# Performance work log

Measured on AMD Instinct MI355X. Metric: run time of the kernel, lower is better.

## Reference

```python
import jax, jax.numpy as jnp
import numpy as np

B, N, E, D = 4, 2048, 2048, 2048  # batch, seq, embedding_dim, out_dim


def setup_inputs() -> dict:
    key = jax.random.key(0)
    k1, k2, k3 = jax.random.split(key, 3)
    x = jax.random.normal(k1, (B, N, E), dtype=jnp.float32)
    # qkv_proj: Linear(E, 3*D). Store weight as [E, 3D] for x @ W.
    W = jax.random.normal(k2, (E, 3 * D), dtype=jnp.float32) * (1.0 / np.sqrt(E))
    b = jax.random.normal(k3, (3 * D,), dtype=jnp.float32) * 0.01
    return {"x": x, "W": W, "b": b}


def reference(x, W, b):
    d = W.shape[1] // 3
    n = x.shape[1]
    qkv = x @ W + b                                   # [B, N, 3D]
    q, k, v = jnp.split(qkv, 3, axis=-1)              # each [B, N, D]
    scale = 1.0 / np.sqrt(d).astype(np.float32)
    att = jnp.einsum('bqd,bkd->bqk', q, k) * scale    # [B, N, N]
    causal = jnp.tril(jnp.ones((n, n), dtype=bool))
    att = jnp.where(causal[None, :, :], att, -jnp.inf)
    # softmax_with_denom: stable softmax, also return the denominator
    m = jnp.max(att, axis=-1, keepdims=True)
    e = jnp.exp(att - m)
    denom = jnp.sum(e, axis=-1)                       # [B, N]
    p = e / denom[..., None]
    y = jnp.einsum('bqk,bkd->bqd', p, v)              # [B, N, D]
    return y, denom
```

## Files before the change

### kernel.cpp

```cpp
#include <hip/hip_runtime.h>

typedef unsigned short u16;
typedef unsigned int   u32;

#define SEQ 2048
#define EMB 2048
#define TD  6144

using bf16x8 = __attribute__((ext_vector_type(8))) __bf16;
using f32x4  = __attribute__((ext_vector_type(4))) float;
using u16x8v = __attribute__((ext_vector_type(8))) u16;

typedef __attribute__((address_space(1))) const void* gas_t;
typedef __attribute__((address_space(3))) void*       las_t;
#define GLOAD16(g, l) __builtin_amdgcn_global_load_lds((gas_t)(g), (las_t)(l), 16, 0, 0)

__device__ __forceinline__ u16 f2bf(float f) {
  u32 u = __float_as_uint(f);
  u += 0x7fffu + ((u >> 16) & 1u);
  return (u16)(u >> 16);
}
__device__ __forceinline__ float bf2f(u16 b) {
  u32 u = (u32)b << 16;
  return __uint_as_float(u);
}

__global__ __launch_bounds__(256) void prep_kern(const float* __restrict__ x,
                                                 u16* __restrict__ xb,
                                                 const float* __restrict__ W,
                                                 u16* __restrict__ Wt) {
  int bid = blockIdx.x;
  int tid = threadIdx.x;
  if (bid < 16384) {
    size_t i = ((size_t)bid * 256 + tid) * 4;
    float4 v = *(const float4*)(x + i);
    ushort4 u;
    u.x = f2bf(v.x); u.y = f2bf(v.y); u.z = f2bf(v.z); u.w = f2bf(v.w);
    *(ushort4*)(xb + i) = u;
  } else {
    __shared__ float t[64][65];
    int wb = bid - 16384;
    int c0 = (wb % 96) * 64, r0 = (wb / 96) * 64;
#pragma unroll
    for (int i = 0; i < 4; ++i) {
      int flat = i * 1024 + tid * 4;
      int r = flat >> 6, c = flat & 63;
      float4 v = *(const float4*)(W + (size_t)(r0 + r) * TD + c0 + c);
      t[r][c] = v.x; t[r][c + 1] = v.y; t[r][c + 2] = v.z; t[r][c + 3] = v.w;
    }
    __syncthreads();
#pragma unroll
    for (int i = 0; i < 4; ++i) {
      int flat = i * 1024 + tid * 4;
      int wr = flat >> 6, wc = flat & 63;
      ushort4 u;
      u.x = f2bf(t[wc + 0][wr]); u.y = f2bf(t[wc + 1][wr]);
      u.z = f2bf(t[wc + 2][wr]); u.w = f2bf(t[wc + 3][wr]);
      *(ushort4*)(Wt + (size_t)(c0 + wr) * EMB + r0 + wc) = u;
    }
  }
}

__global__ __launch_bounds__(512, 2) void gemm_qkv(const u16* __restrict__ Ab,
                                                   const u16* __restrict__ Bb,
                                                   u16* __restrict__ Cb,
                                                   u16* __restrict__ Cb2,
                                                   const float* __restrict__ bias) {
  __shared__ char lds[2][65536];
  constexpr int lda = EMB, ldb = EMB;
  int bid = blockIdx.x;
  int wg = (bid & 7) * 96 + (bid >> 3);
  const u16* A = Ab;
  const u16* Bt = Bb;
  int row0 = (wg / 24) * 256, col0 = (wg % 24) * 256, nk = EMB / 64;

  int tid = threadIdx.x;
  int wave = tid >> 6, lane = tid & 63;
  int wm = wave >> 2, wn = wave & 3;

  int sbase[8];
#pragma unroll
  for (int i = 0; i < 4; ++i) sbase[i] = 32768 + i * 8192 + wave * 1024;
#pragma unroll
  for (int i = 0; i < 4; ++i)
    sbase[4 + i] = i * 4096 + ((wave < 4) ? wave * 1024 : 16384 + (wave - 4) * 1024);

  auto stageb = [&](int bi, int t, int buf) {
    int ob = sbase[bi];
    int obl = ob + lane * 16;
    int row = (obl & 32767) >> 7;
    int cb = obl & 127;
    int c = ((cb ^ ((row & 7) << 4)) >> 1) + t * 64;
    const u16* src = (ob < 32768) ? (A + (size_t)(row0 + row) * lda + c)
                                  : (Bt + (size_t)(col0 + row) * ldb + c);
    GLOAD16(src, (char*)&lds[buf][0] + ob);
  };
  auto ldA = [&](int buf, int rr, int ks) -> bf16x8 {
    int cb = ks * 64 + (lane >> 4) * 16;
    return *(const bf16x8*)&lds[buf][rr * 128 + (cb ^ ((rr & 7) << 4))];
  };
  auto ldB = [&](int buf, int rr, int ks) -> bf16x8 {
    int cb = ks * 64 + (lane >> 4) * 16;
    return *(const bf16x8*)&lds[buf][32768 + rr * 128 + (cb ^ ((rr & 7) << 4))];
  };

  f32x4 acc[8][4];
#pragma unroll
  for (int m = 0; m < 8; ++m)
#pragma unroll
    for (int n = 0; n < 4; ++n) acc[m][n] = (f32x4){0.f, 0.f, 0.f, 0.f};

#pragma unroll
  for (int bi = 0; bi < 8; ++bi) stageb(bi, 0, 0);
#pragma unroll
  for (int bi = 0; bi < 6; ++bi) stageb(bi, 1, 1);
  asm volatile("s_waitcnt vmcnt(6)" ::: "memory");
  __builtin_amdgcn_s_barrier();

  bf16x8 bfg[4][2];
  for (int t = 0; t < nk; ++t) {
    int cur = t & 1, nxt = cur ^ 1;
    bool pf1 = (t + 1 < nk), pf2 = (t + 2 < nk);
    bf16x8 afg[2][2];
#pragma unroll
    for (int n = 0; n < 4; ++n)
#pragma unroll
      for (int ks = 0; ks < 2; ++ks)
        bfg[n][ks] = ldB(cur, wn * 64 + n * 16 + (lane & 15), ks);
#pragma unroll
    for (int m = 0; m < 2; ++m)
#pragma unroll
      for (int ks = 0; ks < 2; ++ks)
        afg[m][ks] = ldA(cur, wm * 128 + m * 16 + (lane & 15), ks);
    if (pf1) { stageb(6, t + 1, nxt); stageb(7, t + 1, nxt); }
    __builtin_amdgcn_s_setprio(1);
#pragma unroll
    for (int m = 0; m < 2; ++m)
#pragma unroll
      for (int n = 0; n < 4; ++n)
#pragma unroll
        for (int ks = 0; ks < 2; ++ks)
          acc[m][n] = __builtin_amdgcn_mfma_f32_16x16x32_bf16(
              afg[m][ks], bfg[n][ks], acc[m][n], 0, 0, 0);
    __builtin_amdgcn_s_setprio(0);
    __builtin_amdgcn_s_barrier();
#pragma unroll
    for (int m = 0; m < 2; ++m)
#pragma unroll
      for (int ks = 0; ks < 2; ++ks)
        afg[m][ks] = ldA(cur, wm * 128 + (2 + m) * 16 + (lane & 15), ks);
    if (pf2) { stageb(0, t + 2, cur); stageb(1, t + 2, cur); }
    __builtin_amdgcn_s_setprio(1);
#pragma unroll
    for (int m = 0; m < 2; ++m)
#pragma unroll
      for (int n = 0; n < 4; ++n)
#pragma unroll
        for (int ks = 0; ks < 2; ++ks)
          acc[2 + m][n] = __builtin_amdgcn_mfma_f32_16x16x32_bf16(
              afg[m][ks], bfg[n][ks], acc[2 + m][n], 0, 0, 0);
    __builtin_amdgcn_s_setprio(0);
#pragma unroll
    for (int m = 0; m < 2; ++m)
#pragma unroll
      for (int ks = 0; ks < 2; ++ks)
        afg[m][ks] = ldA(cur, wm * 128 + (4 + m) * 16 + (lane & 15), ks);
    if (pf2) { stageb(2, t + 2, cur); stageb(3, t + 2, cur); }
    __builtin_amdgcn_s_setprio(1);
#pragma unroll
    for (int m = 0; m < 2; ++m)
#pragma unroll
      for (int n = 0; n < 4; ++n)
#pragma unroll
        for (int ks = 0; ks < 2; ++ks)
          acc[4 + m][n] = __builtin_amdgcn_mfma_f32_16x16x32_bf16(
              afg[m][ks], bfg[n][ks], acc[4 + m][n], 0, 0, 0);
    __builtin_amdgcn_s_setprio(0);
    __builtin_amdgcn_s_barrier();
#pragma unroll
    for (int m = 0; m < 2; ++m)
#pragma unroll
      for (int ks = 0; ks < 2; ++ks)
        afg[m][ks] = ldA(cur, wm * 128 + (6 + m) * 16 + (lane & 15), ks);
    if (pf2) { stageb(4, t + 2, cur); stageb(5, t + 2, cur); }
    __builtin_amdgcn_s_setprio(1);
#pragma unroll
    for (int m = 0; m < 2; ++m)
#pragma unroll
      for (int n = 0; n < 4; ++n)
#pragma unroll
        for (int ks = 0; ks < 2; ++ks)
          acc[6 + m][n] = __builtin_amdgcn_mfma_f32_16x16x32_bf16(
              afg[m][ks], bfg[n][ks], acc[6 + m][n], 0, 0, 0);
    __builtin_amdgcn_s_setprio(0);
    if (pf2)      asm volatile("s_waitcnt vmcnt(6)" ::: "memory");
    else if (pf1) asm volatile("s_waitcnt vmcnt(0)" ::: "memory");
    __builtin_amdgcn_s_barrier();
  }

  int ln = lane & 15;
  int l4 = (lane >> 4) << 2;
  int rb = row0 + wm * 128, cb0 = col0 + wn * 64;
  if (col0 < 4096) {
    u16* C = Cb;
#pragma unroll
    for (int n = 0; n < 4; ++n) {
      float bv = bias[cb0 + n * 16 + ln];
#pragma unroll
      for (int m = 0; m < 8; ++m)
#pragma unroll
        for (int r = 0; r < 4; ++r)
          C[(size_t)(rb + m * 16 + l4 + r) * 4096 + cb0 + n * 16 + ln] =
              f2bf(acc[m][n][r] + bv);
    }
  } else {
    u16* vTb = Cb2 + (size_t)(row0 >> 11) * SEQ * SEQ;
    int nbase = row0 & 2047;
    u16 (*T)[264] = (u16(*)[264])(&lds[0][0]);
    int half = wn >> 1;
    int dloc0 = (wn & 1) * 64;
#pragma unroll
    for (int hh = 0; hh < 2; ++hh) {
      if (half == hh) {
#pragma unroll
        for (int n = 0; n < 4; ++n) {
          float bv = bias[cb0 + n * 16 + ln];
          int dl = dloc0 + n * 16 + ln;
#pragma unroll
          for (int m = 0; m < 8; ++m) {
            int nn = wm * 128 + m * 16 + l4;
#pragma unroll
            for (int r = 0; r < 4; ++r)
              T[dl][nn + r] = f2bf(acc[m][n][r] + bv);
          }
        }
      }
      __syncthreads();
      int dl = tid >> 5, nn = (tid & 31) * 8;
#pragma unroll
      for (int it = 0; it < 8; ++it) {
        int loc = it * 16 + dl;
        *(u16x8v*)&vTb[(size_t)(col0 - 4096 + hh * 128 + loc) * SEQ + nbase + nn] =
            *(const u16x8v*)&T[loc][nn];
      }
      __syncthreads();
    }
  }
}

template <int MODE>
__global__ __launch_bounds__(256, 2) void gemm128(const u16* __restrict__ Ab,
                                                  const u16* __restrict__ Bb,
                                                  void* __restrict__ Cb) {
  __shared__ char lds[2][32768];
  constexpr int lda = 4096;
  constexpr int ldb = (MODE == 1) ? 4096 : SEQ;

  int bid = blockIdx.x;
  const u16 *A, *Bt;
  int row0, col0, nk;
  size_t coff;
  if constexpr (MODE == 1) {
    constexpr int CPX = 544 / 8;
    int wg = (bid & 7) * CPX + (bid >> 3);
    int b = wg / 136, tq = wg % 136;
    int qi = (int)((sqrtf(8.f * (float)tq + 1.f) - 1.f) * 0.5f);
    while ((qi + 1) * (qi + 2) / 2 <= tq) ++qi;
    while (qi * (qi + 1) / 2 > tq) --qi;
    int kj = tq - qi * (qi + 1) / 2;
    A = Ab + (size_t)b * SEQ * 4096;
    Bt = A + 2048;
    row0 = qi * 128; col0 = kj * 128; nk = EMB / 64;
    coff = (size_t)b * SEQ * 4096;
  } else {
    int xcd = bid & 7, idx = bid >> 3;
    int qi = 15 - (idx >> 3);
    int g = xcd * 8 + (idx & 7);
    int b = g >> 4, nj = g & 15;
    A = Ab + (size_t)b * SEQ * 4096;
    Bt = Bb + (size_t)b * SEQ * SEQ;
    row0 = qi * 128; col0 = nj * 128; nk = (qi + 1) * 2;
    coff = (size_t)b * SEQ * SEQ;
  }

  int tid = threadIdx.x;
  int wave = tid >> 6, lane = tid & 63;
  int wm = wave >> 1, wn = wave & 1;
  int ln = lane & 15;

  int sbase[8];
#pragma unroll
  for (int i = 0; i < 4; ++i) sbase[i] = 16384 + i * 4096 + wave * 1024;
#pragma unroll
  for (int i = 0; i < 4; ++i) sbase[4 + i] = i * 4096 + wave * 1024;

  auto stageb = [&](int bi, int t, int buf) {
    int ob = sbase[bi];
    int obl = ob + lane * 16;
    int row = (obl & 16383) >> 7;
    int cb = obl & 127;
    int c = ((cb ^ ((row & 7) << 4)) >> 1) + t * 64;
    const u16* src = (ob < 16384) ? (A + (size_t)(row0 + row) * lda + c)
                                  : (Bt + (size_t)(col0 + row) * ldb + c);
    GLOAD16(src, (char*)&lds[buf][0] + ob);
  };
  auto ldA = [&](int buf, int rr, int ks) -> bf16x8 {
    int cb = ks * 64 + (lane >> 4) * 16;
    return *(const bf16x8*)&lds[buf][rr * 128 + (cb ^ ((rr & 7) << 4))];
  };
  auto ldB = [&](int buf, int rr, int ks) -> bf16x8 {
    int cb = ks * 64 + (lane >> 4) * 16;
    return *(const bf16x8*)&lds[buf][16384 + rr * 128 + (cb ^ ((rr & 7) << 4))];
  };

  f32x4 acc[4][4];
#pragma unroll
  for (int m = 0; m < 4; ++m)
#pragma unroll
    for (int n = 0; n < 4; ++n) acc[m][n] = (f32x4){0.f, 0.f, 0.f, 0.f};

#pragma unroll
  for (int bi = 0; bi < 8; ++bi) stageb(bi, 0, 0);
  stageb(0, 1, 1); stageb(1, 1, 1); stageb(2, 1, 1); stageb(3, 1, 1);
  stageb(4, 1, 1); stageb(6, 1, 1);
  asm volatile("s_waitcnt vmcnt(6)" ::: "memory");
  __builtin_amdgcn_s_barrier();

  bf16x8 bfg[4][2];
  for (int t = 0; t < nk; ++t) {
    int cur = t & 1, nxt = cur ^ 1;
    bool pf1 = (t + 1 < nk), pf2 = (t + 2 < nk);
    bf16x8 afg[2][2];
#pragma unroll
    for (int n = 0; n < 4; ++n)
#pragma unroll
      for (int ks = 0; ks < 2; ++ks)
        bfg[n][ks] = ldB(cur, wn * 64 + n * 16 + ln, ks);
#pragma unroll
    for (int m = 0; m < 2; ++m)
#pragma unroll
      for (int ks = 0; ks < 2; ++ks)
        afg[m][ks] = ldA(cur, wm * 64 + m * 16 + ln, ks);
    if (pf1) { stageb(5, t + 1, nxt); stageb(7, t + 1, nxt); }
    __builtin_amdgcn_s_setprio(1);
#pragma unroll
    for (int m = 0; m < 2; ++m)
#pragma unroll
      for (int n = 0; n < 4; ++n)
#pragma unroll
        for (int ks = 0; ks < 2; ++ks)
          acc[m][n] = __builtin_amdgcn_mfma_f32_16x16x32_bf16(
              afg[m][ks], bfg[n][ks], acc[m][n], 0, 0, 0);
    __builtin_amdgcn_s_setprio(0);
    __builtin_amdgcn_s_barrier();
#pragma unroll
    for (int m = 0; m < 2; ++m)
#pragma unroll
      for (int ks = 0; ks < 2; ++ks)
        afg[m][ks] = ldA(cur, wm * 64 + (2 + m) * 16 + ln, ks);
    if (pf2) {
      stageb(0, t + 2, cur); stageb(1, t + 2, cur); stageb(2, t + 2, cur);
      stageb(3, t + 2, cur); stageb(4, t + 2, cur); stageb(6, t + 2, cur);
    }
    __builtin_amdgcn_s_setprio(1);
#pragma unroll
    for (int m = 0; m < 2; ++m)
#pragma unroll
      for (int n = 0; n < 4; ++n)
#pragma unroll
        for (int ks = 0; ks < 2; ++ks)
          acc[2 + m][n] = __builtin_amdgcn_mfma_f32_16x16x32_bf16(
              afg[m][ks], bfg[n][ks], acc[2 + m][n], 0, 0, 0);
    __builtin_amdgcn_s_setprio(0);
    if (pf2)      asm volatile("s_waitcnt vmcnt(6)" ::: "memory");
    else if (pf1) asm volatile("s_waitcnt vmcnt(0)" ::: "memory");
    __builtin_amdgcn_s_barrier();
  }

  int l4 = (lane >> 4) << 2;
  int rb = row0 + wm * 64, cb0 = col0 + wn * 64;
  if constexpr (MODE == 1) {
    u16* C = (u16*)Cb + coff;
    const float scale = 0.022097086912079608f;
#pragma unroll
    for (int m = 0; m < 4; ++m)
#pragma unroll
      for (int n = 0; n < 4; ++n)
#pragma unroll
        for (int r = 0; r < 4; ++r)
          C[(size_t)(rb + m * 16 + l4 + r) * 4096 + cb0 + n * 16 + ln] =
              f2bf(acc[m][n][r] * scale);
  } else {
    float* C = (float*)Cb + coff;
#pragma unroll
    for (int m = 0; m < 4; ++m)
#pragma unroll
      for (int n = 0; n < 4; ++n)
#pragma unroll
        for (int r = 0; r < 4; ++r)
          C[(size_t)(rb + m * 16 + l4 + r) * SEQ + cb0 + n * 16 + ln] = acc[m][n][r];
  }
}

__global__ __launch_bounds__(256) void softmax_kern(u16* __restrict__ att,
                                                    float* __restrict__ denom) {
  int row = blockIdx.x;
  int q = row & (SEQ - 1);
  u16* arow = att + (size_t)row * 4096;
  int jlen = ((q >> 7) + 1) << 7;
  int tid = threadIdx.x;
  int j0 = tid * 8;
  float NI = -__builtin_inff();
  float a[8];
#pragma unroll
  for (int e = 0; e < 8; ++e) a[e] = NI;
  if (j0 < jlen) {
    u16x8v v = *(const u16x8v*)(arow + j0);
#pragma unroll
    for (int e = 0; e < 8; ++e)
      a[e] = (j0 + e <= q) ? bf2f(v[e]) : NI;
  }
  float mx = a[0];
#pragma unroll
  for (int e = 1; e < 8; ++e) mx = fmaxf(mx, a[e]);
#pragma unroll
  for (int off = 32; off; off >>= 1) mx = fmaxf(mx, __shfl_xor(mx, off, 64));
  __shared__ float red[8];
  int wv = tid >> 6;
  if ((tid & 63) == 0) red[wv] = mx;
  __syncthreads();
  mx = fmaxf(fmaxf(red[0], red[1]), fmaxf(red[2], red[3]));
  float s = 0.f;
#pragma unroll
  for (int e = 0; e < 8; ++e) { a[e] = expf(a[e] - mx); s += a[e]; }
#pragma unroll
  for (int off = 32; off; off >>= 1) s += __shfl_xor(s, off, 64);
  if ((tid & 63) == 0) red[4 + wv] = s;
  __syncthreads();
  s = red[4] + red[5] + red[6] + red[7];
  float inv = 1.0f / s;
  if (j0 < jlen) {
    u16x8v u;
#pragma unroll
    for (int e = 0; e < 8; ++e) u[e] = f2bf(a[e] * inv);
    *(u16x8v*)(arow + j0) = u;
  }
  if (tid == 0) denom[row] = s;
}

extern "C" void kernel_launch(void* const* d_in, const int* in_sizes, int n_in,
                              void* d_out, int out_size, void* d_ws, size_t ws_size,
                              hipStream_t stream) {
  const float* x    = (const float*)d_in[0];
  const float* W    = (const float*)d_in[1];
  const float* bias = (const float*)d_in[2];

  if (ws_size < 201326592u) return;

  char* w = (char*)d_ws;
  u16*   qk  = (u16*)w;
  u16*   vT  = (u16*)(w + 67108864);
  u16*   xb  = (u16*)(w + 100663296);
  u16*   Wt  = (u16*)(w + 134217728);
  u16*   att = (u16*)(w + 134217728);

  float* y     = (float*)d_out;
  float* denom = y + (size_t)4 * SEQ * SEQ;

  prep_kern<<<19456, 256, 0, stream>>>(x, xb, W, Wt);
  gemm_qkv<<<768, 512, 0, stream>>>(xb, Wt, qk, vT, bias);
  gemm128<1><<<544, 256, 0, stream>>>(qk, nullptr, att);
  softmax_kern<<<8192, 256, 0, stream>>>(att, denom);
  gemm128<2><<<1024, 256, 0, stream>>>(att, vT, y);
}
```

Measured before the change: 326.7 us.

## Replace interleaved deep prefetch with simple double-buffered GEMM pipeline

Both GEMM kernels drop the staggered prefetch schedule, which had split the next-next tile loads across compute phases, used mid-loop barriers and waited with vmcnt(6). Each iteration now issues all loads for the next tile at the top, computes the current tile, then waits with vmcnt(0) and hits one barrier. This removes intra-loop barriers and simplifies scheduling. The cost is less memory lookahead, since prefetch distance shrinks to one tile and the full wait may stall.

Result: slower. 342.0 us (+4.7%).

```diff
diff --git a/kernel.cpp b/kernel.cpp
--- a/kernel.cpp
+++ b/kernel.cpp
@@ -112,89 +112,42 @@
 
 #pragma unroll
   for (int bi = 0; bi < 8; ++bi) stageb(bi, 0, 0);
-#pragma unroll
-  for (int bi = 0; bi < 6; ++bi) stageb(bi, 1, 1);
-  asm volatile("s_waitcnt vmcnt(6)" ::: "memory");
+  asm volatile("s_waitcnt vmcnt(0)" ::: "memory");
   __builtin_amdgcn_s_barrier();
 
-  bf16x8 bfg[4][2];
   for (int t = 0; t < nk; ++t) {
     int cur = t & 1, nxt = cur ^ 1;
-    bool pf1 = (t + 1 < nk), pf2 = (t + 2 < nk);
-    bf16x8 afg[2][2];
+    bool pf = (t + 1 < nk);
+    if (pf) {
+#pragma unroll
+      for (int bi = 0; bi < 8; ++bi) stageb(bi, t + 1, nxt);
+    }
+    bf16x8 bfg[4][2];
 #pragma unroll
     for (int n = 0; n < 4; ++n)
 #pragma unroll
       for (int ks = 0; ks < 2; ++ks)
         bfg[n][ks] = ldB(cur, wn * 64 + n * 16 + (lane & 15), ks);
 #pragma unroll
-    for (int m = 0; m < 2; ++m)
-#pragma unroll
-      for (int ks = 0; ks < 2; ++ks)
-        afg[m][ks] = ldA(cur, wm * 128 + m * 16 + (lane & 15), ks);
-    if (pf1) { stageb(6, t + 1, nxt); stageb(7, t + 1, nxt); }
-    __builtin_amdgcn_s_setprio(1);
-#pragma unroll
-    for (int m = 0; m < 2; ++m)
-#pragma unroll
-      for (int n = 0; n < 4; ++n)
+    for (int p = 0; p < 4; ++p) {
+      bf16x8 afg[2][2];
+#pragma unroll
+      for (int m = 0; m < 2; ++m)
 #pragma unroll
         for (int ks = 0; ks < 2; ++ks)
-          acc[m][n] = __builtin_amdgcn_mfma_f32_16x16x32_bf16(
-              afg[m][ks], bfg[n][ks], acc[m][n], 0, 0, 0);
-    __builtin_amdgcn_s_setprio(0);
-    __builtin_amdgcn_s_barrier();
-#pragma unroll
-    for (int m = 0; m < 2; ++m)
-#pragma unroll
-      for (int ks = 0; ks < 2; ++ks)
-        afg[m][ks] = ldA(cur, wm * 128 + (2 + m) * 16 + (lane & 15), ks);
-    if (pf2) { stageb(0, t + 2, cur); stageb(1, t + 2, cur); }
-    __builtin_amdgcn_s_setprio(1);
-#pragma unroll
-    for (int m = 0; m < 2; ++m)
-#pragma unroll
-      for (int n = 0; n < 4; ++n)
-#pragma unroll
-        for (int ks = 0; ks < 2; ++ks)
-          acc[2 + m][n] = __builtin_amdgcn_mfma_f32_16x16x32_bf16(
-              afg[m][ks], bfg[n][ks], acc[2 + m][n], 0, 0, 0);
-    __builtin_amdgcn_s_setprio(0);
-#pragma unroll
-    for (int m = 0; m < 2; ++m)
-#pragma unroll
-      for (int ks = 0; ks < 2; ++ks)
-        afg[m][ks] = ldA(cur, wm * 128 + (4 + m) * 16 + (lane & 15), ks);
-    if (pf2) { stageb(2, t + 2, cur); stageb(3, t + 2, cur); }
-    __builtin_amdgcn_s_setprio(1);
-#pragma unroll
-    for (int m = 0; m < 2; ++m)
-#pragma unroll
-      for (int n = 0; n < 4; ++n)
-#pragma unroll
-        for (int ks = 0; ks < 2; ++ks)
-          acc[4 + m][n] = __builtin_amdgcn_mfma_f32_16x16x32_bf16(
-              afg[m][ks], bfg[n][ks], acc[4 + m][n], 0, 0, 0);
-    __builtin_amdgcn_s_setprio(0);
-    __builtin_amdgcn_s_barrier();
-#pragma unroll
-    for (int m = 0; m < 2; ++m)
-#pragma unroll
-      for (int ks = 0; ks < 2; ++ks)
-        afg[m][ks] = ldA(cur, wm * 128 + (6 + m) * 16 + (lane & 15), ks);
-    if (pf2) { stageb(4, t + 2, cur); stageb(5, t + 2, cur); }
-    __builtin_amdgcn_s_setprio(1);
-#pragma unroll
-    for (int m = 0; m < 2; ++m)
-#pragma unroll
-      for (int n = 0; n < 4; ++n)
-#pragma unroll
-        for (int ks = 0; ks < 2; ++ks)
-          acc[6 + m][n] = __builtin_amdgcn_mfma_f32_16x16x32_bf16(
-              afg[m][ks], bfg[n][ks], acc[6 + m][n], 0, 0, 0);
-    __builtin_amdgcn_s_setprio(0);
-    if (pf2)      asm volatile("s_waitcnt vmcnt(6)" ::: "memory");
-    else if (pf1) asm volatile("s_waitcnt vmcnt(0)" ::: "memory");
+          afg[m][ks] = ldA(cur, wm * 128 + (p * 2 + m) * 16 + (lane & 15), ks);
+      __builtin_amdgcn_s_setprio(1);
+#pragma unroll
+      for (int m = 0; m < 2; ++m)
+#pragma unroll
+        for (int n = 0; n < 4; ++n)
+#pragma unroll
+          for (int ks = 0; ks < 2; ++ks)
+            acc[p * 2 + m][n] = __builtin_amdgcn_mfma_f32_16x16x32_bf16(
+                afg[m][ks], bfg[n][ks], acc[p * 2 + m][n], 0, 0, 0);
+      __builtin_amdgcn_s_setprio(0);
+    }
+    if (pf) asm volatile("s_waitcnt vmcnt(0)" ::: "memory");
     __builtin_amdgcn_s_barrier();
   }
 
@@ -321,59 +274,42 @@
 
 #pragma unroll
   for (int bi = 0; bi < 8; ++bi) stageb(bi, 0, 0);
-  stageb(0, 1, 1); stageb(1, 1, 1); stageb(2, 1, 1); stageb(3, 1, 1);
-  stageb(4, 1, 1); stageb(6, 1, 1);
-  asm volatile("s_waitcnt vmcnt(6)" ::: "memory");
+  asm volatile("s_waitcnt vmcnt(0)" ::: "memory");
   __builtin_amdgcn_s_barrier();
 
-  bf16x8 bfg[4][2];
   for (int t = 0; t < nk; ++t) {
     int cur = t & 1, nxt = cur ^ 1;
-    bool pf1 = (t + 1 < nk), pf2 = (t + 2 < nk);
-    bf16x8 afg[2][2];
+    bool pf = (t + 1 < nk);
+    if (pf) {
+#pragma unroll
+      for (int bi = 0; bi < 8; ++bi) stageb(bi, t + 1, nxt);
+    }
+    bf16x8 bfg[4][2];
 #pragma unroll
     for (int n = 0; n < 4; ++n)
 #pragma unroll
       for (int ks = 0; ks < 2; ++ks)
         bfg[n][ks] = ldB(cur, wn * 64 + n * 16 + ln, ks);
 #pragma unroll
-    for (int m = 0; m < 2; ++m)
-#pragma unroll
-      for (int ks = 0; ks < 2; ++ks)
-        afg[m][ks] = ldA(cur, wm * 64 + m * 16 + ln, ks);
-    if (pf1) { stageb(5, t + 1, nxt); stageb(7, t + 1, nxt); }
-    __builtin_amdgcn_s_setprio(1);
-#pragma unroll
-    for (int m = 0; m < 2; ++m)
-#pragma unroll
-      for (int n = 0; n < 4; ++n)
+    for (int p = 0; p < 2; ++p) {
+      bf16x8 afg[2][2];
+#pragma unroll
+      for (int m = 0; m < 2; ++m)
 #pragma unroll
         for (int ks = 0; ks < 2; ++ks)
-          acc[m][n] = __builtin_amdgcn_mfma_f32_16x16x32_bf16(
-              afg[m][ks], bfg[n][ks], acc[m][n], 0, 0, 0);
-    __builtin_amdgcn_s_setprio(0);
-    __builtin_amdgcn_s_barrier();
-#pragma unroll
-    for (int m = 0; m < 2; ++m)
-#pragma unroll
-      for (int ks = 0; ks < 2; ++ks)
-        afg[m][ks] = ldA(cur, wm * 64 + (2 + m) * 16 + ln, ks);
-    if (pf2) {
-      stageb(0, t + 2, cur); stageb(1, t + 2, cur); stageb(2, t + 2, cur);
-      stageb(3, t + 2, cur); stageb(4, t + 2, cur); stageb(6, t + 2, cur);
-    }
-    __builtin_amdgcn_s_setprio(1);
-#pragma unroll
-    for (int m = 0; m < 2; ++m)
-#pragma unroll
-      for (int n = 0; n < 4; ++n)
-#pragma unroll
-        for (int ks = 0; ks < 2; ++ks)
-          acc[2 + m][n] = __builtin_amdgcn_mfma_f32_16x16x32_bf16(
-              afg[m][ks], bfg[n][ks], acc[2 + m][n], 0, 0, 0);
-    __builtin_amdgcn_s_setprio(0);
-    if (pf2)      asm volatile("s_waitcnt vmcnt(6)" ::: "memory");
-    else if (pf1) asm volatile("s_waitcnt vmcnt(0)" ::: "memory");
+          afg[m][ks] = ldA(cur, wm * 64 + (p * 2 + m) * 16 + ln, ks);
+      __builtin_amdgcn_s_setprio(1);
+#pragma unroll
+      for (int m = 0; m < 2; ++m)
+#pragma unroll
+        for (int n = 0; n < 4; ++n)
+#pragma unroll
+          for (int ks = 0; ks < 2; ++ks)
+            acc[p * 2 + m][n] = __builtin_amdgcn_mfma_f32_16x16x32_bf16(
+                afg[m][ks], bfg[n][ks], acc[p * 2 + m][n], 0, 0, 0);
+      __builtin_amdgcn_s_setprio(0);
+    }
+    if (pf) asm volatile("s_waitcnt vmcnt(0)" ::: "memory");
     __builtin_amdgcn_s_barrier();
   }
 
```

## Halve K-tile to 32 and shrink LDS to raise gemm occupancy

Applied to the files above, without the earlier changes.

Changes the gemm128 kernel's K step from 64 to 32, halving the LDS double buffer to 2x16KB, and raises launch bounds to allow up to 5 blocks per CU. The staging layout and swizzle are reworked so 64-wide swizzled rows hold two K-halves of different rows. The goal is more resident workgroups to hide memory latency. In exchange there are twice as many loop iterations and barriers, each with less MFMA work, and register pressure is tighter under the new bound.

New measurement: 440.1 us. 34.7% more time.

```diff
diff --git a/kernel.cpp b/kernel.cpp
--- a/kernel.cpp
+++ b/kernel.cpp
@@ -249,10 +249,10 @@
 }
 
 template <int MODE>
-__global__ __launch_bounds__(256, 2) void gemm128(const u16* __restrict__ Ab,
+__global__ __launch_bounds__(256, 5) void gemm128(const u16* __restrict__ Ab,
                                                   const u16* __restrict__ Bb,
                                                   void* __restrict__ Cb) {
-  __shared__ char lds[2][32768];
+  __shared__ char lds[2][16384];
   constexpr int lda = 4096;
   constexpr int ldb = (MODE == 1) ? 4096 : SEQ;
 
@@ -270,7 +270,7 @@
     int kj = tq - qi * (qi + 1) / 2;
     A = Ab + (size_t)b * SEQ * 4096;
     Bt = A + 2048;
-    row0 = qi * 128; col0 = kj * 128; nk = EMB / 64;
+    row0 = qi * 128; col0 = kj * 128; nk = EMB / 32;
     coff = (size_t)b * SEQ * 4096;
   } else {
     int xcd = bid & 7, idx = bid >> 3;
@@ -279,7 +279,7 @@
     int b = g >> 4, nj = g & 15;
     A = Ab + (size_t)b * SEQ * 4096;
     Bt = Bb + (size_t)b * SEQ * SEQ;
-    row0 = qi * 128; col0 = nj * 128; nk = (qi + 1) * 2;
+    row0 = qi * 128; col0 = nj * 128; nk = (qi + 1) * 4;
     coff = (size_t)b * SEQ * SEQ;
   }
 
@@ -288,30 +288,23 @@
   int wm = wave >> 1, wn = wave & 1;
   int ln = lane & 15;
 
-  int sbase[8];
-#pragma unroll
-  for (int i = 0; i < 4; ++i) sbase[i] = 16384 + i * 4096 + wave * 1024;
-#pragma unroll
-  for (int i = 0; i < 4; ++i) sbase[4 + i] = i * 4096 + wave * 1024;
-
   auto stageb = [&](int bi, int t, int buf) {
-    int ob = sbase[bi];
-    int obl = ob + lane * 16;
-    int row = (obl & 16383) >> 7;
-    int cb = obl & 127;
-    int c = ((cb ^ ((row & 7) << 4)) >> 1) + t * 64;
-    const u16* src = (ob < 16384) ? (A + (size_t)(row0 + row) * lda + c)
-                                  : (Bt + (size_t)(col0 + row) * ldb + c);
-    GLOAD16(src, (char*)&lds[buf][0] + ob);
+    int off0 = (bi < 2) ? 8192 + bi * 4096 : (bi - 2) * 4096;
+    int local = tid * 16;
+    int L = ((bi & 1) ? 32 : 0) + (local >> 7);
+    int ro = local & 127;
+    int rop = ro ^ ((L & 7) << 4);
+    int r = L + (rop >> 6) * 64;
+    int c = ((rop & 63) >> 1) + t * 32;
+    const u16* src = (bi < 2) ? (Bt + (size_t)(col0 + r) * ldb + c)
+                              : (A + (size_t)(row0 + r) * lda + c);
+    GLOAD16(src, (char*)&lds[buf][0] + off0 + wave * 1024);
   };
-  auto ldA = [&](int buf, int rr, int ks) -> bf16x8 {
-    int cb = ks * 64 + (lane >> 4) * 16;
-    return *(const bf16x8*)&lds[buf][rr * 128 + (cb ^ ((rr & 7) << 4))];
+  auto ldfrag = [&](const char* base, int r) -> bf16x8 {
+    int L = r & 63, h = r >> 6;
+    int off = (h * 64 + (lane >> 4) * 16) ^ ((L & 7) << 4);
+    return *(const bf16x8*)(base + L * 128 + off);
   };
-  auto ldB = [&](int buf, int rr, int ks) -> bf16x8 {
-    int cb = ks * 64 + (lane >> 4) * 16;
-    return *(const bf16x8*)&lds[buf][16384 + rr * 128 + (cb ^ ((rr & 7) << 4))];
-  };
 
   f32x4 acc[4][4];
 #pragma unroll
@@ -320,59 +313,43 @@
     for (int n = 0; n < 4; ++n) acc[m][n] = (f32x4){0.f, 0.f, 0.f, 0.f};
 
 #pragma unroll
-  for (int bi = 0; bi < 8; ++bi) stageb(bi, 0, 0);
-  stageb(0, 1, 1); stageb(1, 1, 1); stageb(2, 1, 1); stageb(3, 1, 1);
-  stageb(4, 1, 1); stageb(6, 1, 1);
-  asm volatile("s_waitcnt vmcnt(6)" ::: "memory");
+  for (int bi = 0; bi < 4; ++bi) stageb(bi, 0, 0);
+  stageb(0, 1, 1); stageb(1, 1, 1); stageb(2, 1, 1);
+  asm volatile("s_waitcnt vmcnt(3)" ::: "memory");
   __builtin_amdgcn_s_barrier();
 
-  bf16x8 bfg[4][2];
   for (int t = 0; t < nk; ++t) {
     int cur = t & 1, nxt = cur ^ 1;
     bool pf1 = (t + 1 < nk), pf2 = (t + 2 < nk);
-    bf16x8 afg[2][2];
-#pragma unroll
-    for (int n = 0; n < 4; ++n)
-#pragma unroll
-      for (int ks = 0; ks < 2; ++ks)
-        bfg[n][ks] = ldB(cur, wn * 64 + n * 16 + ln, ks);
-#pragma unroll
-    for (int m = 0; m < 2; ++m)
-#pragma unroll
-      for (int ks = 0; ks < 2; ++ks)
-        afg[m][ks] = ldA(cur, wm * 64 + m * 16 + ln, ks);
-    if (pf1) { stageb(5, t + 1, nxt); stageb(7, t + 1, nxt); }
-    __builtin_amdgcn_s_setprio(1);
-#pragma unroll
-    for (int m = 0; m < 2; ++m)
-#pragma unroll
-      for (int n = 0; n < 4; ++n)
-#pragma unroll
-        for (int ks = 0; ks < 2; ++ks)
-          acc[m][n] = __builtin_amdgcn_mfma_f32_16x16x32_bf16(
-              afg[m][ks], bfg[n][ks], acc[m][n], 0, 0, 0);
+    const char* Ab_ = &lds[cur][0];
+    const char* Bb_ = &lds[cur][8192];
+    bf16x8 bfg[4], afg[2];
+#pragma unroll
+    for (int n = 0; n < 4; ++n) bfg[n] = ldfrag(Bb_, wn * 64 + n * 16 + ln);
+#pragma unroll
+    for (int m = 0; m < 2; ++m) afg[m] = ldfrag(Ab_, wm * 64 + m * 16 + ln);
+    if (pf1) stageb(3, t + 1, nxt);
+    __builtin_amdgcn_s_setprio(1);
+#pragma unroll
+    for (int m = 0; m < 2; ++m)
+#pragma unroll
+      for (int n = 0; n < 4; ++n)
+        acc[m][n] = __builtin_amdgcn_mfma_f32_16x16x32_bf16(
+            afg[m], bfg[n], acc[m][n], 0, 0, 0);
     __builtin_amdgcn_s_setprio(0);
     __builtin_amdgcn_s_barrier();
 #pragma unroll
-    for (int m = 0; m < 2; ++m)
-#pragma unroll
-      for (int ks = 0; ks < 2; ++ks)
-        afg[m][ks] = ldA(cur, wm * 64 + (2 + m) * 16 + ln, ks);
-    if (pf2) {
-      stageb(0, t + 2, cur); stageb(1, t + 2, cur); stageb(2, t + 2, cur);
-      stageb(3, t + 2, cur); stageb(4, t + 2, cur); stageb(6, t + 2, cur);
-    }
-    __builtin_amdgcn_s_setprio(1);
-#pragma unroll
-    for (int m = 0; m < 2; ++m)
-#pragma unroll
-      for (int n = 0; n < 4; ++n)
-#pragma unroll
-        for (int ks = 0; ks < 2; ++ks)
-          acc[2 + m][n] = __builtin_amdgcn_mfma_f32_16x16x32_bf16(
-              afg[m][ks], bfg[n][ks], acc[2 + m][n], 0, 0, 0);
-    __builtin_amdgcn_s_setprio(0);
-    if (pf2)      asm volatile("s_waitcnt vmcnt(6)" ::: "memory");
+    for (int m = 0; m < 2; ++m) afg[m] = ldfrag(Ab_, wm * 64 + (2 + m) * 16 + ln);
+    if (pf2) { stageb(0, t + 2, cur); stageb(1, t + 2, cur); stageb(2, t + 2, cur); }
+    __builtin_amdgcn_s_setprio(1);
+#pragma unroll
+    for (int m = 0; m < 2; ++m)
+#pragma unroll
+      for (int n = 0; n < 4; ++n)
+        acc[2 + m][n] = __builtin_amdgcn_mfma_f32_16x16x32_bf16(
+            afg[m], bfg[n], acc[2 + m][n], 0, 0, 0);
+    __builtin_amdgcn_s_setprio(0);
+    if (pf2)      asm volatile("s_waitcnt vmcnt(3)" ::: "memory");
     else if (pf1) asm volatile("s_waitcnt vmcnt(0)" ::: "memory");
     __builtin_amdgcn_s_barrier();
   }
```
